# Kernel optimization log

Hardware: AMD Instinct MI355X
Metric: run time of the kernel (lower is better)

Reference implementation:

```python
import jax, jax.numpy as jnp
import numpy as np

N_AGENTS = 8
STATE_DIM = 256
NODE = 2 * N_AGENTS          # 16 graph nodes per sample
FEAT = STATE_DIM // NODE     # 16
NHID = 4
NHEADS = 4
GOUT = 2 * FEAT              # 32 = gat_output
EMBED = 32                   # mixing_embed_dim
ALPHA = 0.2                  # leaky relu slope in GAT
LAYER_IN = NODE * GOUT       # 512 = state_dim * 2
BS = 2048
T = 128


def setup_inputs() -> dict:
    key = jax.random.key(0)
    ks = jax.random.split(key, 16)
    r = lambda i, shape: jax.random.normal(ks[i], shape, dtype=jnp.float32) * 0.1
    return dict(
        agent_qs=jax.random.normal(ks[0], (BS, T, N_AGENTS), dtype=jnp.float32),
        states=jax.random.normal(ks[1], (BS, T, STATE_DIM), dtype=jnp.float32),
        # GAT params: 4 attention heads + output attention layer
        W_heads=r(2, (NHEADS, FEAT, NHID)),
        a_heads=r(3, (NHEADS, 2 * NHID, 1)),
        W_out=r(4, (NHEADS * NHID, GOUT)),
        a_out=r(5, (2 * GOUT, 1)),
        # hypernet params (torch Linear stored as [in, out])
        hw1_w=r(6, (LAYER_IN, EMBED * N_AGENTS)), hw1_b=r(7, (EMBED * N_AGENTS,)),
        hb1_w=r(8, (LAYER_IN, EMBED)), hb1_b=r(9, (EMBED,)),
        hwf_w=r(10, (LAYER_IN, EMBED)), hwf_b=r(11, (EMBED,)),
        v1_w=r(12, (LAYER_IN, EMBED)), v1_b=r(13, (EMBED,)),
        v2_w=r(14, (EMBED, 1)), v2_b=r(15, (1,)),
    )


def _gat_layer(x, W, a, concat):
    # Standard pyGAT GraphAttentionLayer; adj is all-ones so no masking needed.
    Wh = x @ W                       # [N, F']
    Fo = W.shape[1]
    e1 = Wh @ a[:Fo]                 # [N, 1]
    e2 = Wh @ a[Fo:]                 # [N, 1]
    e = jax.nn.leaky_relu(e1 + e2.T, ALPHA)  # [N, N]
    att = jax.nn.softmax(e, axis=1)
    h = att @ Wh                     # [N, F']
    return jax.nn.elu(h) if concat else h


def _gat(x, W_heads, a_heads, W_out, a_out):
    # x: [NODE, FEAT] -> [NODE, GOUT]; dropout is identity (eval mode)
    heads = jax.vmap(lambda W, a: _gat_layer(x, W, a, True))(W_heads, a_heads)  # [H, N, NHID]
    h = jnp.transpose(heads, (1, 0, 2)).reshape(x.shape[0], NHEADS * NHID)      # concat heads
    return jax.nn.elu(_gat_layer(h, W_out, a_out, False))


def reference(agent_qs, states, W_heads, a_heads, W_out, a_out,
              hw1_w, hw1_b, hb1_w, hb1_b, hwf_w, hwf_b,
              v1_w, v1_b, v2_w, v2_b):
    bs, t = agent_qs.shape[0], agent_qs.shape[1]
    nodes = states.reshape(bs * t, NODE, FEAT)
    # batched GAT over all (batch*time) tiny graphs (replaces Python loops)
    gat = jax.vmap(lambda x: _gat(x, W_heads, a_heads, W_out, a_out))(nodes)  # [bt, N, GOUT]
    s = gat.reshape(bs * t, LAYER_IN)
    qs = agent_qs.reshape(bs * t, 1, N_AGENTS)
    # QMIX mixing with hypernetworks
    w1 = jnp.abs(s @ hw1_w + hw1_b).reshape(-1, N_AGENTS, EMBED)
    b1 = (s @ hb1_w + hb1_b).reshape(-1, 1, EMBED)
    hidden = jax.nn.elu(jnp.einsum('bij,bjk->bik', qs, w1) + b1)  # [bt, 1, EMBED]
    w_final = jnp.abs(s @ hwf_w + hwf_b).reshape(-1, EMBED, 1)
    v = (jax.nn.relu(s @ v1_w + v1_b) @ v2_w + v2_b).reshape(-1, 1, 1)
    y = jnp.einsum('bij,bjk->bik', hidden, w_final) + v          # [bt, 1, 1]
    return y.reshape(bs, t, 1)
```

## Files before the change

### kernel.cpp

```cpp
#include <hip/hip_runtime.h>
#include <hip/hip_bf16.h>
#include <stdint.h>


#define BT       (2048 * 128)
#define ALPHA    0.2f
#define NTILE    22
#define KSTEPS   16
#define AUXOFF   360448

typedef __attribute__((ext_vector_type(8))) short bf16x8;
typedef __attribute__((ext_vector_type(4))) float f32x4;
typedef __attribute__((ext_vector_type(2))) float f32x2;
typedef _Float16 f16x2 __attribute__((ext_vector_type(2)));

__device__ __forceinline__ f32x2 b2(float s) { return (f32x2){s, s}; }
__device__ __forceinline__ f32x2 pkfma(f32x2 a, f32x2 b, f32x2 c) {
    return __builtin_elementwise_fma(a, b, c);
}
__device__ __forceinline__ float elu1(float x) { return x > 0.f ? x : (__expf(x) - 1.f); }

__device__ __forceinline__ unsigned short f32_to_bf16_rne(float x) {
    uint32_t u = __float_as_uint(x);
    u += 0x7fffu + ((u >> 16) & 1u);
    return (unsigned short)(u >> 16);
}

__device__ __forceinline__ float fdot2f(uint32_t a, f16x2 b, float c) {
#if __has_builtin(__builtin_amdgcn_fdot2)
    return __builtin_amdgcn_fdot2(__builtin_bit_cast(f16x2, a), b, c, false);
#else
    const f16x2 av = __builtin_bit_cast(f16x2, a);
    return fmaf((float)av.x, (float)b.x, fmaf((float)av.y, (float)b.y, c));
#endif
}
__device__ __forceinline__ f16x2 pkrtz(float a, float b) {
    return __builtin_bit_cast(f16x2, __builtin_amdgcn_cvt_pkrtz(a, b));
}
__device__ __forceinline__ uint32_t cvtpk_bf16(float lo, float hi) {
    uint32_t r;
    asm("v_cvt_pk_bf16_f32 %0, %1, %2" : "=v"(r) : "v"(lo), "v"(hi));
    return r;
}

__device__ __forceinline__ f32x2 softmax16p(const float* e2A, const float* e2B,
                                            f32x2 e1, f32x2* ee) {
    #pragma unroll
    for (int t4 = 0; t4 < 4; ++t4) {
        const float4 va = *(const float4*)&e2A[t4 * 4];
        const float4 vb = *(const float4*)&e2B[t4 * 4];
        const f32x2 l0 = e1 + (f32x2){va.x, vb.x};
        const f32x2 l1 = e1 + (f32x2){va.y, vb.y};
        const f32x2 l2 = e1 + (f32x2){va.z, vb.z};
        const f32x2 l3 = e1 + (f32x2){va.w, vb.w};
        ee[4*t4+0] = __builtin_elementwise_max(l0, l0 * b2(ALPHA));
        ee[4*t4+1] = __builtin_elementwise_max(l1, l1 * b2(ALPHA));
        ee[4*t4+2] = __builtin_elementwise_max(l2, l2 * b2(ALPHA));
        ee[4*t4+3] = __builtin_elementwise_max(l3, l3 * b2(ALPHA));
    }
    f32x2 m0 = __builtin_elementwise_max(ee[0], ee[1]);
    f32x2 m1 = __builtin_elementwise_max(ee[2], ee[3]);
    f32x2 m2 = __builtin_elementwise_max(ee[4], ee[5]);
    f32x2 m3 = __builtin_elementwise_max(ee[6], ee[7]);
    f32x2 m4 = __builtin_elementwise_max(ee[8], ee[9]);
    f32x2 m5 = __builtin_elementwise_max(ee[10], ee[11]);
    f32x2 m6 = __builtin_elementwise_max(ee[12], ee[13]);
    f32x2 m7 = __builtin_elementwise_max(ee[14], ee[15]);
    m0 = __builtin_elementwise_max(m0, m1); m2 = __builtin_elementwise_max(m2, m3);
    m4 = __builtin_elementwise_max(m4, m5); m6 = __builtin_elementwise_max(m6, m7);
    const f32x2 mx = __builtin_elementwise_max(__builtin_elementwise_max(m0, m2),
                                               __builtin_elementwise_max(m4, m6));
    #pragma unroll
    for (int j = 0; j < 16; ++j) {
        const f32x2 d = ee[j] - mx;
        ee[j] = (f32x2){__expf(d.x), __expf(d.y)};
    }
    f32x2 s0 = ee[0]+ee[1], s1 = ee[2]+ee[3], s2 = ee[4]+ee[5], s3 = ee[6]+ee[7];
    f32x2 s4 = ee[8]+ee[9], s5 = ee[10]+ee[11], s6 = ee[12]+ee[13], s7 = ee[14]+ee[15];
    s0 += s1; s2 += s3; s4 += s5; s6 += s7;
    const f32x2 sum = (s0 + s2) + (s4 + s6);
    return (f32x2){__builtin_amdgcn_rcpf(sum.x), __builtin_amdgcn_rcpf(sum.y)};
}

__global__ __launch_bounds__(256) void pack_b(
    const float* __restrict__ hw1_w, const float* __restrict__ hb1_w,
    const float* __restrict__ hwf_w, const float* __restrict__ v1_w,
    const float* __restrict__ W_out, const float* __restrict__ a_out,
    unsigned short* __restrict__ bpack, float* __restrict__ aux)
{
    const int gi = blockIdx.x * 256 + threadIdx.x;
    if (gi < KSTEPS * NTILE * 64) {
        const int l  = gi & 63;
        const int ni = (gi >> 6) % NTILE;
        const int kt = gi / (NTILE * 64);
        const int col = ni * 16 + (l & 15);
        const int k0  = kt * 32 + (l >> 4) * 8;
        const float* src; int stride; int c;
        if (col < 256)      { src = hw1_w; stride = 256; c = col; }
        else if (col < 288) { src = hb1_w; stride = 32;  c = col - 256; }
        else if (col < 320) { src = hwf_w; stride = 32;  c = col - 288; }
        else                { src = v1_w;  stride = 32;  c = col - 320; }
        union { unsigned short u[8]; uint4 v; } pk;
        #pragma unroll
        for (int e = 0; e < 8; ++e) pk.u[e] = f32_to_bf16_rne(src[(long)(k0 + e) * stride + c]);
        ((uint4*)bpack)[gi] = pk.v;
    } else if (gi < KSTEPS * NTILE * 64 + 32) {
        const int a = gi - KSTEPS * NTILE * 64;
        const int which = a >> 4, f = a & 15;
        float s = 0.f;
        for (int c = 0; c < 32; ++c) s = fmaf(W_out[f * 32 + c], a_out[which * 32 + c], s);
        aux[a] = s;
    }
}

__global__ __launch_bounds__(256) void fused_kernel(
    const float* __restrict__ agent_qs, const float* __restrict__ states,
    const float* __restrict__ W_heads,  const float* __restrict__ a_heads,
    const float* __restrict__ W_out,    const float* __restrict__ a_out,
    const unsigned short* __restrict__ bpack, const float* __restrict__ aux,
    const float* __restrict__ hw1_b, const float* __restrict__ hb1_b,
    const float* __restrict__ hwf_b, const float* __restrict__ v1_b,
    const float* __restrict__ v2_w,  const float* __restrict__ v2_b,
    float* __restrict__ out)
{
    __shared__ unsigned short A[32][512];
    __shared__ float bst[384];
    __shared__ float qs[288];
    __shared__ float ysum[4][4][4];

    const int t    = threadIdx.x;
    const int w    = t >> 6;
    const int lane = t & 63;
    const int g    = lane >> 4;
    const int n    = lane & 15;
    const long sbase = (long)blockIdx.x * 32;

    char* scr = (char*)&A[0][0] + w * 8192;
    _Float16* hxA = (_Float16*)(scr + (g * 2)     * 528);
    _Float16* hxB = (_Float16*)(scr + (g * 2 + 1) * 528);
    float*    e2A = (float*)(scr + 4224 + (g * 2)     * 80);
    float*    e2B = (float*)(scr + 4224 + (g * 2 + 1) * 80);

    const int mA = w * 8 + g;
    const int mB = w * 8 + 4 + g;

    f32x2 xr2[16];
    {
        const float4* xa = (const float4*)(states + (sbase + mA) * 256 + n * 16);
        const float4* xb = (const float4*)(states + (sbase + mB) * 256 + n * 16);
        #pragma unroll
        for (int i = 0; i < 4; ++i) {
            const float4 va = xa[i], vb = xb[i];
            xr2[4*i+0] = (f32x2){va.x, vb.x};
            xr2[4*i+1] = (f32x2){va.y, vb.y};
            xr2[4*i+2] = (f32x2){va.z, vb.z};
            xr2[4*i+3] = (f32x2){va.w, vb.w};
        }
    }

    f32x2 hcat2[16];
    #pragma unroll
    for (int h = 0; h < 4; ++h) {
        f32x2 wh0 = b2(0.f), wh1 = b2(0.f), wh2 = b2(0.f), wh3 = b2(0.f);
        #pragma unroll
        for (int f = 0; f < 16; ++f) {
            const f32x2 xf = xr2[f];
            wh0 = pkfma(xf, b2(W_heads[h*64 + f*4 + 0]), wh0);
            wh1 = pkfma(xf, b2(W_heads[h*64 + f*4 + 1]), wh1);
            wh2 = pkfma(xf, b2(W_heads[h*64 + f*4 + 2]), wh2);
            wh3 = pkfma(xf, b2(W_heads[h*64 + f*4 + 3]), wh3);
        }
        const f32x2 e1 = pkfma(wh0, b2(a_heads[h*8+0]),
                         pkfma(wh1, b2(a_heads[h*8+1]),
                         pkfma(wh2, b2(a_heads[h*8+2]), wh3 * b2(a_heads[h*8+3]))));
        const f32x2 e2 = pkfma(wh0, b2(a_heads[h*8+4]),
                         pkfma(wh1, b2(a_heads[h*8+5]),
                         pkfma(wh2, b2(a_heads[h*8+6]), wh3 * b2(a_heads[h*8+7]))));
        hxA[0*16 + n] = (_Float16)wh0.x;  hxB[0*16 + n] = (_Float16)wh0.y;
        hxA[1*16 + n] = (_Float16)wh1.x;  hxB[1*16 + n] = (_Float16)wh1.y;
        hxA[2*16 + n] = (_Float16)wh2.x;  hxB[2*16 + n] = (_Float16)wh2.y;
        hxA[3*16 + n] = (_Float16)wh3.x;  hxB[3*16 + n] = (_Float16)wh3.y;
        e2A[n] = e2.x;
        e2B[n] = e2.y;

        f32x2 ee[16];
        const f32x2 inv = softmax16p(e2A, e2B, e1, ee);
        f16x2 eA[8], eB[8];
        #pragma unroll
        for (int jp = 0; jp < 8; ++jp) {
            eA[jp] = pkrtz(ee[2*jp].x, ee[2*jp+1].x);
            eB[jp] = pkrtz(ee[2*jp].y, ee[2*jp+1].y);
        }
        #pragma unroll
        for (int k = 0; k < 4; ++k) {
            const uint4 wa0 = *(const uint4*)&hxA[k*16];
            const uint4 wa1 = *(const uint4*)&hxA[k*16 + 8];
            const uint4 wb0 = *(const uint4*)&hxB[k*16];
            const uint4 wb1 = *(const uint4*)&hxB[k*16 + 8];
            float sA = 0.f, sB = 0.f;
            sA = fdot2f(wa0.x, eA[0], sA);  sB = fdot2f(wb0.x, eB[0], sB);
            sA = fdot2f(wa0.y, eA[1], sA);  sB = fdot2f(wb0.y, eB[1], sB);
            sA = fdot2f(wa0.z, eA[2], sA);  sB = fdot2f(wb0.z, eB[2], sB);
            sA = fdot2f(wa0.w, eA[3], sA);  sB = fdot2f(wb0.w, eB[3], sB);
            sA = fdot2f(wa1.x, eA[4], sA);  sB = fdot2f(wb1.x, eB[4], sB);
            sA = fdot2f(wa1.y, eA[5], sA);  sB = fdot2f(wb1.y, eB[5], sB);
            sA = fdot2f(wa1.z, eA[6], sA);  sB = fdot2f(wb1.z, eB[6], sB);
            sA = fdot2f(wa1.w, eA[7], sA);  sB = fdot2f(wb1.w, eB[7], sB);
            hcat2[h*4+k] = (f32x2){elu1(sA * inv.x), elu1(sB * inv.y)};
        }
    }

    f32x2 e1o = b2(0.f), e2o = b2(0.f);
    #pragma unroll
    for (int f = 0; f < 16; ++f) {
        e1o = pkfma(hcat2[f], b2(aux[f]), e1o);
        e2o = pkfma(hcat2[f], b2(aux[16 + f]), e2o);
    }
    #pragma unroll
    for (int f = 0; f < 16; ++f) {
        hxA[f*16 + n] = (_Float16)hcat2[f].x;
        hxB[f*16 + n] = (_Float16)hcat2[f].y;
    }
    e2A[n] = e2o.x;
    e2B[n] = e2o.y;

    f32x2 ee[16];
    const f32x2 invo = softmax16p(e2A, e2B, e1o, ee);
    f16x2 eA[8], eB[8];
    #pragma unroll
    for (int jp = 0; jp < 8; ++jp) {
        eA[jp] = pkrtz(ee[2*jp].x, ee[2*jp+1].x);
        eB[jp] = pkrtz(ee[2*jp].y, ee[2*jp+1].y);
    }
    f32x2 hagg[16];
    #pragma unroll
    for (int f = 0; f < 16; ++f) {
        const uint4 wa0 = *(const uint4*)&hxA[f*16];
        const uint4 wa1 = *(const uint4*)&hxA[f*16 + 8];
        const uint4 wb0 = *(const uint4*)&hxB[f*16];
        const uint4 wb1 = *(const uint4*)&hxB[f*16 + 8];
        float sA = 0.f, sB = 0.f;
        sA = fdot2f(wa0.x, eA[0], sA);  sB = fdot2f(wb0.x, eB[0], sB);
        sA = fdot2f(wa0.y, eA[1], sA);  sB = fdot2f(wb0.y, eB[1], sB);
        sA = fdot2f(wa0.z, eA[2], sA);  sB = fdot2f(wb0.z, eB[2], sB);
        sA = fdot2f(wa0.w, eA[3], sA);  sB = fdot2f(wb0.w, eB[3], sB);
        sA = fdot2f(wa1.x, eA[4], sA);  sB = fdot2f(wb1.x, eB[4], sB);
        sA = fdot2f(wa1.y, eA[5], sA);  sB = fdot2f(wb1.y, eB[5], sB);
        sA = fdot2f(wa1.z, eA[6], sA);  sB = fdot2f(wb1.z, eB[6], sB);
        sA = fdot2f(wa1.w, eA[7], sA);  sB = fdot2f(wb1.w, eB[7], sB);
        hagg[f] = (f32x2){sA, sB} * invo;
    }
    #pragma unroll 1
    for (int hf = 0; hf < 2; ++hf) {
        f32x2 gh[16];
        #pragma unroll
        for (int c = 0; c < 16; ++c) gh[c] = b2(0.f);
        #pragma unroll
        for (int f = 0; f < 16; ++f) {
            const f32x2 hv = hagg[f];
            #pragma unroll
            for (int c = 0; c < 16; ++c)
                gh[c] = pkfma(hv, b2(W_out[f*32 + hf*16 + c]), gh[c]);
        }
        #pragma unroll
        for (int k2 = 0; k2 < 2; ++k2) {
            const int kq = hf * 2 + k2;
            float vA[8], vB[8];
            #pragma unroll
            for (int i2 = 0; i2 < 8; ++i2) {
                vA[i2] = elu1(gh[k2*8 + i2].x);
                vB[i2] = elu1(gh[k2*8 + i2].y);
            }
            uint4 pA, pB;
            pA.x = cvtpk_bf16(vA[0], vA[1]); pA.y = cvtpk_bf16(vA[2], vA[3]);
            pA.z = cvtpk_bf16(vA[4], vA[5]); pA.w = cvtpk_bf16(vA[6], vA[7]);
            pB.x = cvtpk_bf16(vB[0], vB[1]); pB.y = cvtpk_bf16(vB[2], vB[3]);
            pB.z = cvtpk_bf16(vB[4], vB[5]); pB.w = cvtpk_bf16(vB[6], vB[7]);
            const int chunkA = (kq * 16 + n + mA) & 63;
            const int chunkB = (kq * 16 + n + mB) & 63;
            *(uint4*)((char*)&A[0][0] + mA * 1024 + chunkA * 16) = pA;
            *(uint4*)((char*)&A[0][0] + mB * 1024 + chunkB * 16) = pB;
        }
    }

    __syncthreads();

    const float bv0 = hw1_b[t];
    float bv1 = 0.f;
    if (t < 32)       bv1 = hb1_b[t];
    else if (t < 64)  bv1 = hwf_b[t - 32];
    else if (t < 96)  bv1 = v1_b[t - 64];
    else if (t < 128) bv1 = v2_w[t - 96];
    const float qv = agent_qs[sbase * 8 + t];

    const int mi  = w >> 1;
    const int pr  = w & 1;
    const int arow = mi * 16 + n;

    f32x4 acc[11];
    #pragma unroll
    for (int j = 0; j < 11; ++j) acc[j] = (f32x4){0.f, 0.f, 0.f, 0.f};

    const uint4* Bb = (const uint4*)bpack + lane;
    for (int kt = 0; kt < KSTEPS; ++kt) {
        const int chunk = (g * 16 + kt + arow) & 63;
        bf16x8 af = *(const bf16x8*)((const char*)&A[0][0] + arow * 1024 + chunk * 16);
        const uint4* bp = Bb + (kt * NTILE + pr) * 64;
        #pragma unroll
        for (int j = 0; j < 11; ++j) {
            uint4 bw = bp[(2 * j) * 64];
            bf16x8 bf;
            memcpy(&bf, &bw, 16);
            acc[j] = __builtin_amdgcn_mfma_f32_16x16x32_bf16(af, bf, acc[j], 0, 0, 0);
        }
    }

    bst[t] = bv0;
    if (t < 128) bst[256 + t] = bv1;
    qs[(t >> 3) * 9 + (t & 7)] = qv;
    __syncthreads();

    const int e = pr * 16 + n;
    float yp[4];
    #pragma unroll
    for (int r = 0; r < 4; ++r) {
        const int ms = mi * 16 + g * 4 + r;
        float hs = acc[8][r] + bst[256 + e];
        #pragma unroll
        for (int a = 0; a < 8; ++a)
            hs = fmaf(qs[ms * 9 + a], fabsf(acc[a][r] + bst[a * 32 + e]), hs);
        const float hid = elu1(hs);
        yp[r] = hid * fabsf(acc[9][r] + bst[288 + e])
              + fmaxf(acc[10][r] + bst[320 + e], 0.f) * bst[352 + e];
    }
    #pragma unroll
    for (int mask = 1; mask <= 8; mask <<= 1) {
        #pragma unroll
        for (int r = 0; r < 4; ++r) yp[r] += __shfl_xor(yp[r], mask);
    }
    if (n == 0) {
        #pragma unroll
        for (int r = 0; r < 4; ++r) ysum[w][g][r] = yp[r];
    }
    __syncthreads();

    if (t < 32) {
        const int mi2 = t >> 4, g2 = (t >> 2) & 3, r2 = t & 3;
        out[sbase + t] = ysum[mi2 * 2][g2][r2] + ysum[mi2 * 2 + 1][g2][r2] + v2_b[0];
    }
}

extern "C" void kernel_launch(void* const* d_in, const int* in_sizes, int n_in,
                              void* d_out, int out_size, void* d_ws, size_t ws_size,
                              hipStream_t stream) {
    const float* agent_qs = (const float*)d_in[0];
    const float* states   = (const float*)d_in[1];
    const float* W_heads  = (const float*)d_in[2];
    const float* a_heads  = (const float*)d_in[3];
    const float* W_out    = (const float*)d_in[4];
    const float* a_out    = (const float*)d_in[5];
    const float* hw1_w    = (const float*)d_in[6];
    const float* hw1_b    = (const float*)d_in[7];
    const float* hb1_w    = (const float*)d_in[8];
    const float* hb1_b    = (const float*)d_in[9];
    const float* hwf_w    = (const float*)d_in[10];
    const float* hwf_b    = (const float*)d_in[11];
    const float* v1_w     = (const float*)d_in[12];
    const float* v1_b     = (const float*)d_in[13];
    const float* v2_w     = (const float*)d_in[14];
    const float* v2_b     = (const float*)d_in[15];

    unsigned short* bpack = (unsigned short*)d_ws;
    float* aux = (float*)((char*)d_ws + AUXOFF);

    pack_b<<<(KSTEPS * NTILE * 64 + 32 + 255) / 256, 256, 0, stream>>>(
        hw1_w, hb1_w, hwf_w, v1_w, W_out, a_out, bpack, aux);
    fused_kernel<<<BT / 32, 256, 0, stream>>>(agent_qs, states,
                                              W_heads, a_heads, W_out, a_out,
                                              bpack, aux,
                                              hw1_b, hb1_b, hwf_b, v1_b, v2_w, v2_b,
                                              (float*)d_out);
}
```

Measured before the change: 336.8 us.

## Compute GAT output layer aggregation and projection with bf16 MFMA

Replaces the per-thread fp16 dot-product attention aggregation and scalar packed-FMA W_out projection in the GAT output layer with two chained 32x32x16 bf16 MFMA passes per group. Node features and normalized attention weights are staged in LDS scratch as bf16, and the intermediate result is shuffled across half-waves to form the B operand. The row permutation of the hypernet weight packing is changed to match the new A-tile layout. This aims to cut VALU work and register pressure, at the cost of lower precision (bf16 instead of fp16/fp32) and extra shuffles and LDS traffic.

```diff
diff --git a/kernel.cpp b/kernel.cpp
--- a/kernel.cpp
+++ b/kernel.cpp
@@ -11,6 +11,7 @@
 
 typedef __attribute__((ext_vector_type(8))) short bf16x8;
 typedef __attribute__((ext_vector_type(4))) float f32x4;
+typedef __attribute__((ext_vector_type(16))) float f32x16;
 typedef __attribute__((ext_vector_type(2))) float f32x2;
 typedef _Float16 f16x2 __attribute__((ext_vector_type(2)));
 
@@ -40,6 +41,12 @@
 __device__ __forceinline__ uint32_t cvtpk_bf16(float lo, float hi) {
     uint32_t r;
     asm("v_cvt_pk_bf16_f32 %0, %1, %2" : "=v"(r) : "v"(lo), "v"(hi));
+    return r;
+}
+__device__ __forceinline__ f32x16 z16() {
+    f32x16 r;
+    #pragma unroll
+    for (int i = 0; i < 16; ++i) r[i] = 0.f;
     return r;
 }
 
@@ -102,7 +109,11 @@
         else                { src = v1_w;  stride = 32;  c = col - 320; }
         union { unsigned short u[8]; uint4 v; } pk;
         #pragma unroll
-        for (int e = 0; e < 8; ++e) pk.u[e] = f32_to_bf16_rne(src[(long)(k0 + e) * stride + c]);
+        for (int e = 0; e < 8; ++e) {
+            const int i = k0 + e;
+            const int r_old = ((i & 15) << 5) + (i >> 4);
+            pk.u[e] = f32_to_bf16_rne(src[(long)r_old * stride + c]);
+        }
         ((uint4*)bpack)[gi] = pk.v;
     } else if (gi < KSTEPS * NTILE * 64 + 32) {
         const int a = gi - KSTEPS * NTILE * 64;
@@ -216,71 +227,107 @@
         e1o = pkfma(hcat2[f], b2(aux[f]), e1o);
         e2o = pkfma(hcat2[f], b2(aux[16 + f]), e2o);
     }
-    #pragma unroll
-    for (int f = 0; f < 16; ++f) {
-        hxA[f*16 + n] = (_Float16)hcat2[f].x;
-        hxB[f*16 + n] = (_Float16)hcat2[f].y;
-    }
     e2A[n] = e2o.x;
     e2B[n] = e2o.y;
-
     f32x2 ee[16];
     const f32x2 invo = softmax16p(e2A, e2B, e1o, ee);
-    f16x2 eA[8], eB[8];
-    #pragma unroll
-    for (int jp = 0; jp < 8; ++jp) {
-        eA[jp] = pkrtz(ee[2*jp].x, ee[2*jp+1].x);
-        eB[jp] = pkrtz(ee[2*jp].y, ee[2*jp+1].y);
-    }
-    f32x2 hagg[16];
-    #pragma unroll
-    for (int f = 0; f < 16; ++f) {
-        const uint4 wa0 = *(const uint4*)&hxA[f*16];
-        const uint4 wa1 = *(const uint4*)&hxA[f*16 + 8];
-        const uint4 wb0 = *(const uint4*)&hxB[f*16];
-        const uint4 wb1 = *(const uint4*)&hxB[f*16 + 8];
-        float sA = 0.f, sB = 0.f;
-        sA = fdot2f(wa0.x, eA[0], sA);  sB = fdot2f(wb0.x, eB[0], sB);
-        sA = fdot2f(wa0.y, eA[1], sA);  sB = fdot2f(wb0.y, eB[1], sB);
-        sA = fdot2f(wa0.z, eA[2], sA);  sB = fdot2f(wb0.z, eB[2], sB);
-        sA = fdot2f(wa0.w, eA[3], sA);  sB = fdot2f(wb0.w, eB[3], sB);
-        sA = fdot2f(wa1.x, eA[4], sA);  sB = fdot2f(wb1.x, eB[4], sB);
-        sA = fdot2f(wa1.y, eA[5], sA);  sB = fdot2f(wb1.y, eB[5], sB);
-        sA = fdot2f(wa1.z, eA[6], sA);  sB = fdot2f(wb1.z, eB[6], sB);
-        sA = fdot2f(wa1.w, eA[7], sA);  sB = fdot2f(wb1.w, eB[7], sB);
-        hagg[f] = (f32x2){sA, sB} * invo;
-    }
+    #pragma unroll
+    for (int j = 0; j < 16; ++j) ee[j] *= invo;
+
+    {
+        uint32_t hA[8], hB[8], aAv[8], aBv[8];
+        #pragma unroll
+        for (int p2 = 0; p2 < 8; ++p2) {
+            hA[p2]  = cvtpk_bf16(hcat2[2*p2].x, hcat2[2*p2+1].x);
+            hB[p2]  = cvtpk_bf16(hcat2[2*p2].y, hcat2[2*p2+1].y);
+            aAv[p2] = cvtpk_bf16(ee[2*p2].x, ee[2*p2+1].x);
+            aBv[p2] = cvtpk_bf16(ee[2*p2].y, ee[2*p2+1].y);
+        }
+        char* hb = scr + g * 1024;
+        char* ab = scr + (4 + g) * 1024;
+        uint4 v;
+        v.x=hA[0]; v.y=hA[1]; v.z=hA[2]; v.w=hA[3];  *(uint4*)(hb + n*32)       = v;
+        v.x=hA[4]; v.y=hA[5]; v.z=hA[6]; v.w=hA[7];  *(uint4*)(hb + n*32 + 16)  = v;
+        v.x=hB[0]; v.y=hB[1]; v.z=hB[2]; v.w=hB[3];  *(uint4*)(hb + 512 + n*32) = v;
+        v.x=hB[4]; v.y=hB[5]; v.z=hB[6]; v.w=hB[7];  *(uint4*)(hb + 512 + n*32 + 16) = v;
+        v.x=aAv[0];v.y=aAv[1];v.z=aAv[2];v.w=aAv[3]; *(uint4*)(ab + n*32)       = v;
+        v.x=aAv[4];v.y=aAv[5];v.z=aAv[6];v.w=aAv[7]; *(uint4*)(ab + n*32 + 16)  = v;
+        v.x=aBv[0];v.y=aBv[1];v.z=aBv[2];v.w=aBv[3]; *(uint4*)(ab + 512 + n*32) = v;
+        v.x=aBv[4];v.y=aBv[5];v.z=aBv[6];v.w=aBv[7]; *(uint4*)(ab + 512 + n*32 + 16) = v;
+    }
+
+    const int row  = lane & 31;
+    const int half = lane >> 5;
+    bf16x8 wf;
+    {
+        union { uint32_t d[4]; bf16x8 v; } u;
+        #pragma unroll
+        for (int e = 0; e < 4; ++e)
+            u.d[e] = cvtpk_bf16(W_out[(half*8 + 2*e)*32 + row],
+                                W_out[(half*8 + 2*e + 1)*32 + row]);
+        wf = u.v;
+    }
+
     #pragma unroll 1
-    for (int hf = 0; hf < 2; ++hf) {
-        f32x2 gh[16];
-        #pragma unroll
-        for (int c = 0; c < 16; ++c) gh[c] = b2(0.f);
-        #pragma unroll
-        for (int f = 0; f < 16; ++f) {
-            const f32x2 hv = hagg[f];
-            #pragma unroll
-            for (int c = 0; c < 16; ++c)
-                gh[c] = pkfma(hv, b2(W_out[f*32 + hf*16 + c]), gh[c]);
-        }
-        #pragma unroll
-        for (int k2 = 0; k2 < 2; ++k2) {
-            const int kq = hf * 2 + k2;
-            float vA[8], vB[8];
-            #pragma unroll
-            for (int i2 = 0; i2 < 8; ++i2) {
-                vA[i2] = elu1(gh[k2*8 + i2].x);
-                vB[i2] = elu1(gh[k2*8 + i2].y);
-            }
-            uint4 pA, pB;
-            pA.x = cvtpk_bf16(vA[0], vA[1]); pA.y = cvtpk_bf16(vA[2], vA[3]);
-            pA.z = cvtpk_bf16(vA[4], vA[5]); pA.w = cvtpk_bf16(vA[6], vA[7]);
-            pB.x = cvtpk_bf16(vB[0], vB[1]); pB.y = cvtpk_bf16(vB[2], vB[3]);
-            pB.z = cvtpk_bf16(vB[4], vB[5]); pB.w = cvtpk_bf16(vB[6], vB[7]);
-            const int chunkA = (kq * 16 + n + mA) & 63;
-            const int chunkB = (kq * 16 + n + mB) & 63;
-            *(uint4*)((char*)&A[0][0] + mA * 1024 + chunkA * 16) = pA;
-            *(uint4*)((char*)&A[0][0] + mB * 1024 + chunkB * 16) = pB;
-        }
+    for (int gg = 0; gg < 4; ++gg) {
+        const char* hb = scr + gg * 1024;
+        const char* ab = scr + (4 + gg) * 1024;
+        uint4 af1u = *(const uint4*)(hb + (row & 15) * 32 + (row >> 4) * 512 + half * 16);
+        bf16x8 af1; memcpy(&af1, &af1u, 16);
+        f32x16 D1 = __builtin_amdgcn_mfma_f32_32x32x16_bf16(af1, wf, z16(), 0, 0, 0);
+
+        const uint32_t d0 = cvtpk_bf16(D1[0], D1[1]),   d1 = cvtpk_bf16(D1[2], D1[3]);
+        const uint32_t d2 = cvtpk_bf16(D1[4], D1[5]),   d3 = cvtpk_bf16(D1[6], D1[7]);
+        const uint32_t f0 = cvtpk_bf16(D1[8], D1[9]),   f1 = cvtpk_bf16(D1[10], D1[11]);
+        const uint32_t f2 = cvtpk_bf16(D1[12], D1[13]), f3 = cvtpk_bf16(D1[14], D1[15]);
+        const uint32_t x0 = (uint32_t)__shfl_xor((int)d0, 32);
+        const uint32_t x1 = (uint32_t)__shfl_xor((int)d1, 32);
+        const uint32_t x2 = (uint32_t)__shfl_xor((int)d2, 32);
+        const uint32_t x3 = (uint32_t)__shfl_xor((int)d3, 32);
+        const uint32_t y0 = (uint32_t)__shfl_xor((int)f0, 32);
+        const uint32_t y1 = (uint32_t)__shfl_xor((int)f1, 32);
+        const uint32_t y2 = (uint32_t)__shfl_xor((int)f2, 32);
+        const uint32_t y3 = (uint32_t)__shfl_xor((int)f3, 32);
+        union { uint32_t d[4]; bf16x8 v; } b1u, b2u;
+        if (half == 0) {
+            b1u.d[0]=d0; b1u.d[1]=d1; b1u.d[2]=x0; b1u.d[3]=x1;
+            b2u.d[0]=f0; b2u.d[1]=f1; b2u.d[2]=y0; b2u.d[3]=y1;
+        } else {
+            b1u.d[0]=x2; b1u.d[1]=x3; b1u.d[2]=d2; b1u.d[3]=d3;
+            b2u.d[0]=y2; b2u.d[1]=y3; b2u.d[2]=f2; b2u.d[3]=f3;
+        }
+
+        uint4 aau = {0,0,0,0}, abu = {0,0,0,0};
+        if (row < 16) aau = *(const uint4*)(ab + row * 32 + half * 16);
+        else          abu = *(const uint4*)(ab + 512 + (row - 16) * 32 + half * 16);
+        bf16x8 aaf, abf; memcpy(&aaf, &aau, 16); memcpy(&abf, &abu, 16);
+        f32x16 D2 = __builtin_amdgcn_mfma_f32_32x32x16_bf16(aaf, b1u.v, z16(), 0, 0, 0);
+        D2 = __builtin_amdgcn_mfma_f32_32x32x16_bf16(abf, b2u.v, D2, 0, 0, 0);
+
+        const int c = row;
+        const int mAg = w * 8 + gg, mBg = w * 8 + 4 + gg;
+        const uint32_t pA0 = cvtpk_bf16(elu1(D2[0]),  elu1(D2[1]));
+        const uint32_t pA1 = cvtpk_bf16(elu1(D2[2]),  elu1(D2[3]));
+        const uint32_t pA2 = cvtpk_bf16(elu1(D2[4]),  elu1(D2[5]));
+        const uint32_t pA3 = cvtpk_bf16(elu1(D2[6]),  elu1(D2[7]));
+        const uint32_t pB0 = cvtpk_bf16(elu1(D2[8]),  elu1(D2[9]));
+        const uint32_t pB1 = cvtpk_bf16(elu1(D2[10]), elu1(D2[11]));
+        const uint32_t pB2 = cvtpk_bf16(elu1(D2[12]), elu1(D2[13]));
+        const uint32_t pB3 = cvtpk_bf16(elu1(D2[14]), elu1(D2[15]));
+        const int u0 = 2 * c, u1 = 2 * c + 1;
+        const int pa0 = (((u0 & 3) << 4) + (u0 >> 2) + mAg) & 63;
+        const int pa1 = (((u1 & 3) << 4) + (u1 >> 2) + mAg) & 63;
+        const int pb0 = (((u0 & 3) << 4) + (u0 >> 2) + mBg) & 63;
+        const int pb1 = (((u1 & 3) << 4) + (u1 >> 2) + mBg) & 63;
+        uint2 wv;
+        wv.x = pA0; wv.y = pA1;
+        *(uint2*)((char*)&A[0][0] + mAg * 1024 + pa0 * 16 + half * 8) = wv;
+        wv.x = pA2; wv.y = pA3;
+        *(uint2*)((char*)&A[0][0] + mAg * 1024 + pa1 * 16 + half * 8) = wv;
+        wv.x = pB0; wv.y = pB1;
+        *(uint2*)((char*)&A[0][0] + mBg * 1024 + pb0 * 16 + half * 8) = wv;
+        wv.x = pB2; wv.y = pB3;
+        *(uint2*)((char*)&A[0][0] + mBg * 1024 + pb1 * 16 + half * 8) = wv;
     }
 
     __syncthreads();
```

Measured after the change: 293.2 us. 1.15x faster.
